# Kernel optimization log

Hardware: AMD Instinct MI355X
Metric: run time of the kernel (lower is better)

## Reference

```python
import jax, jax.numpy as jnp
import numpy as np

N_EMBD = 1024
N_HEAD = 16
HEAD = N_EMBD // N_HEAD


def setup_inputs() -> dict:
    key = jax.random.key(0)
    ks = jax.random.split(key, 6)
    B, S = 4, 2048
    scale = 1.0 / np.sqrt(N_EMBD)
    return {
        "x": jax.random.normal(ks[0], (B, S, N_EMBD), dtype=jnp.float32),
        "Wq": jax.random.normal(ks[1], (N_EMBD, N_EMBD), dtype=jnp.float32) * scale,
        "Wk": jax.random.normal(ks[2], (N_EMBD, N_EMBD), dtype=jnp.float32) * scale,
        "Wv": jax.random.normal(ks[3], (N_EMBD, N_EMBD), dtype=jnp.float32) * scale,
        "Wo": jax.random.normal(ks[4], (N_EMBD, N_EMBD), dtype=jnp.float32) * scale,
        "bo": jnp.zeros((N_EMBD,), dtype=jnp.float32),
    }


def reference(x, Wq, Wk, Wv, Wo, bo):
    B, S, _ = x.shape
    # projections; nn.Linear applies x @ W.T but W is random here, so x @ W is equivalent math
    def split_heads(t):  # (B,S,E) -> (B,H,S,D)
        return t.reshape(B, S, N_HEAD, HEAD).transpose(0, 2, 1, 3)

    q = split_heads(x @ Wq)
    k = split_heads(x @ Wk)
    v = split_heads(x @ Wv)
    scores = jnp.einsum("bhqd,bhkd->bhqk", q, k) * (HEAD ** -0.5)
    causal = jnp.tril(jnp.ones((S, S), dtype=bool))
    scores = jnp.where(causal, scores, -jnp.inf)
    weights = jax.nn.softmax(scores, axis=-1)  # dropout p=0 (eval)
    out = jnp.einsum("bhqk,bhkd->bhqd", weights, v)
    out = out.transpose(0, 2, 1, 3).reshape(B, S, N_EMBD)
    return out @ Wo + bo
```

## Files before the change

### kernel.cpp

```cpp
#include <hip/hip_runtime.h>
#include <hip/hip_bf16.h>

typedef unsigned short u16;
typedef unsigned int u32;
typedef __bf16 bf16x8 __attribute__((ext_vector_type(8)));
typedef float f32x4 __attribute__((ext_vector_type(4)));
typedef u16 u16x8 __attribute__((ext_vector_type(8)));
typedef u16 u16x4 __attribute__((ext_vector_type(4)));

#define NB 4
#define SEQ 2048
#define EMB 1024
#define NHEAD 16
#define DHEAD 64
#define MTOT (NB*SEQ)

static __device__ __forceinline__ u16 f2bf(float f) {
  union { __bf16 h; u16 u; } cv;
  cv.h = (__bf16)f;
  return cv.u;
}

static __device__ __forceinline__ float fexp2(float x) {
  float r;
  asm("v_exp_f32 %0, %1" : "=v"(r) : "v"(x));
  return r;
}

static __device__ __forceinline__ void gload16(const void* g, void* l) {
  __builtin_amdgcn_global_load_lds((const __attribute__((address_space(1))) void*)g,
                                   (__attribute__((address_space(3))) void*)l, 16, 0, 0);
}


__global__ __launch_bounds__(256) void k_cvt_x(const float* __restrict__ in, u16* __restrict__ out) {
  size_t i = (size_t)blockIdx.x * 256 + threadIdx.x;
  const float4* p = (const float4*)in + i * 2;
  float4 a = p[0], b = p[1];
  u16x8 r;
  r[0] = f2bf(a.x); r[1] = f2bf(a.y); r[2] = f2bf(a.z); r[3] = f2bf(a.w);
  r[4] = f2bf(b.x); r[5] = f2bf(b.y); r[6] = f2bf(b.z); r[7] = f2bf(b.w);
  *(u16x8*)(out + i * 8) = r;
}

__global__ __launch_bounds__(256) void k_wtrans(const float* __restrict__ W0, const float* __restrict__ W1,
                                                const float* __restrict__ W2, const float* __restrict__ W3,
                                                u16* __restrict__ O0, u16* __restrict__ O1,
                                                u16* __restrict__ O2, u16* __restrict__ O3) {
  __shared__ float tile[64][65];
  const float* W = blockIdx.z == 0 ? W0 : blockIdx.z == 1 ? W1 : blockIdx.z == 2 ? W2 : W3;
  u16* O       = blockIdx.z == 0 ? O0 : blockIdx.z == 1 ? O1 : blockIdx.z == 2 ? O2 : O3;
  const int c0 = blockIdx.x * 64, r0 = blockIdx.y * 64;
  const int t = threadIdx.x;
  const int tr = t >> 4, tc = (t & 15) * 4;
#pragma unroll
  for (int p = 0; p < 4; p++) {
    int r = tr + p * 16;
    float4 v = *(const float4*)&W[(size_t)(r0 + r) * EMB + c0 + tc];
    tile[r][tc + 0] = v.x; tile[r][tc + 1] = v.y; tile[r][tc + 2] = v.z; tile[r][tc + 3] = v.w;
  }
  __syncthreads();
#pragma unroll
  for (int p = 0; p < 4; p++) {
    int orow = tr + p * 16;
    u16x4 o;
    o[0] = f2bf(tile[tc + 0][orow]); o[1] = f2bf(tile[tc + 1][orow]);
    o[2] = f2bf(tile[tc + 2][orow]); o[3] = f2bf(tile[tc + 3][orow]);
    *(u16x4*)&O[(size_t)(c0 + orow) * EMB + r0 + tc] = o;
  }
}


static __device__ __forceinline__ void gemm_core(const u16* __restrict__ A, const u16* __restrict__ BT,
                                                 int m0, int n0, f32x4 acc[4][4]) {
  __shared__ u16 As[2][128 * 64];
  __shared__ u16 Bs[2][128 * 64];
  const int t = threadIdx.x, l = t & 63, w = t >> 6;
  const int g = l >> 4, q = l & 15;
  const int wm = (w >> 1) * 64, wn = (w & 1) * 64;

  const f32x4 zero4 = {0.f, 0.f, 0.f, 0.f};
#pragma unroll
  for (int mi = 0; mi < 4; mi++)
#pragma unroll
    for (int ni = 0; ni < 4; ni++) acc[mi][ni] = zero4;

  int srow[4], skel[4];
#pragma unroll
  for (int i = 0; i < 4; i++) {
    int row = w * 32 + i * 8 + (l >> 3);
    srow[i] = row; skel[i] = ((l & 7) ^ (row & 7)) * 8;
  }

  auto stage = [&](int k0, int bsel) {
    char* AsB = (char*)As[bsel] + w * 4096;
    char* BsB = (char*)Bs[bsel] + w * 4096;
#pragma unroll
    for (int i = 0; i < 4; i++) {
      gload16(A + (size_t)(m0 + srow[i]) * EMB + k0 + skel[i], AsB + i * 1024);
      gload16(BT + (size_t)(n0 + srow[i]) * EMB + k0 + skel[i], BsB + i * 1024);
    }
  };

  auto compute = [&](int bsel) {
    char* AsB = (char*)As[bsel];
    char* BsB = (char*)Bs[bsel];
#pragma unroll
    for (int kc = 0; kc < 2; kc++) {
      bf16x8 af[4], bfv[4];
#pragma unroll
      for (int mi = 0; mi < 4; mi++) {
        int row = wm + mi * 16 + q;
        af[mi] = *(const bf16x8*)(AsB + row * 128 + (((kc * 4 + g) ^ (row & 7)) << 4));
      }
#pragma unroll
      for (int ni = 0; ni < 4; ni++) {
        int row = wn + ni * 16 + q;
        bfv[ni] = *(const bf16x8*)(BsB + row * 128 + (((kc * 4 + g) ^ (row & 7)) << 4));
      }
      __builtin_amdgcn_s_setprio(1);
#pragma unroll
      for (int mi = 0; mi < 4; mi++)
#pragma unroll
        for (int ni = 0; ni < 4; ni++)
          acc[mi][ni] = __builtin_amdgcn_mfma_f32_16x16x32_bf16(af[mi], bfv[ni], acc[mi][ni], 0, 0, 0);
      __builtin_amdgcn_s_setprio(0);
    }
  };

  stage(0, 0);
  int buf = 0;
  for (int k0 = 64; k0 <= EMB; k0 += 64) {
    const bool pf = (k0 < EMB);
    if (pf) {
      stage(k0, buf ^ 1);
      asm volatile("s_waitcnt vmcnt(8)" ::: "memory");
    } else {
      asm volatile("s_waitcnt vmcnt(0)" ::: "memory");
    }
    __builtin_amdgcn_s_barrier();
    __builtin_amdgcn_sched_barrier(0);
    compute(buf);
    asm volatile("s_waitcnt lgkmcnt(0)" ::: "memory");
    __builtin_amdgcn_s_barrier();
    buf ^= 1;
  }
}

__global__ __launch_bounds__(512, 2) void k_gemm_qkv(const u16* __restrict__ xb, const u16* __restrict__ Wqkv,
                                                     u16* __restrict__ Qb, u16* __restrict__ Kb, u16* __restrict__ Vb) {
  __shared__ u16 As[2][256 * 64];
  __shared__ u16 Bs[2][256 * 64];
  const int t = threadIdx.x, l = t & 63, wid = t >> 6;
  const int g = l >> 4, q = l & 15;
  const int wr = wid >> 2, wc = wid & 3;

  const int wg = blockIdx.x;
  const int c = wg & 7, local = wg >> 3;
  const int idx = c * 48 + local;
  const int ni_ = idx >> 5, mi_ = idx & 31;
  const int m0 = mi_ * 256, n0 = ni_ * 256;

  f32x4 acc[2][2][4][2];
  const f32x4 zero4 = {0.f, 0.f, 0.f, 0.f};
#pragma unroll
  for (int R = 0; R < 2; R++)
#pragma unroll
    for (int C = 0; C < 2; C++)
#pragma unroll
      for (int mi = 0; mi < 4; mi++)
#pragma unroll
        for (int ni = 0; ni < 2; ni++) acc[R][C][mi][ni] = zero4;

  int srow[2], skel[2];
#pragma unroll
  for (int j = 0; j < 2; j++) {
    int row = j * 64 + (t >> 3);
    srow[j] = row; skel[j] = ((t & 7) ^ (row & 7)) * 8;
  }

  auto stageHalf = [&](int op, int half, int tile) {
    if (tile >= 16) return;
    const int kk = tile * 64, d = tile & 1;
    const u16* src = op ? Wqkv : xb;
    const int base = op ? n0 : m0;
    char* dst = (char*)(op ? Bs[d] : As[d]) + half * 16384 + wid * 1024;
#pragma unroll
    for (int j = 0; j < 2; j++)
      gload16(src + (size_t)(base + half * 128 + srow[j]) * EMB + kk + skel[j], dst + j * 8192);
  };

  bf16x8 af[4][2], bf0[2][2], bf1[2][2];
  auto loadA = [&](int R, int d) {
    char* Ab = (char*)As[d];
#pragma unroll
    for (int mi = 0; mi < 4; mi++)
#pragma unroll
      for (int kc = 0; kc < 2; kc++) {
        int row = R * 128 + wr * 64 + mi * 16 + q;
        af[mi][kc] = *(const bf16x8*)(Ab + row * 128 + (((kc * 4 + g) ^ (row & 7)) << 4));
      }
  };
  auto loadB = [&](int C, int d, bf16x8 (&bfv)[2][2]) {
    char* Bb = (char*)Bs[d];
#pragma unroll
    for (int ni = 0; ni < 2; ni++)
#pragma unroll
      for (int kc = 0; kc < 2; kc++) {
        int row = C * 128 + wc * 32 + ni * 16 + q;
        bfv[ni][kc] = *(const bf16x8*)(Bb + row * 128 + (((kc * 4 + g) ^ (row & 7)) << 4));
      }
  };

#define MFMA16(R, C, BF)                                                                   \
  do {                                                                                     \
    __builtin_amdgcn_s_setprio(1);                                                         \
    _Pragma("unroll")                                                                      \
    for (int kc = 0; kc < 2; kc++)                                                         \
      _Pragma("unroll")                                                                    \
      for (int mi = 0; mi < 4; mi++)                                                       \
        _Pragma("unroll")                                                                  \
        for (int ni = 0; ni < 2; ni++)                                                     \
          acc[R][C][mi][ni] = __builtin_amdgcn_mfma_f32_16x16x32_bf16(af[mi][kc], BF[ni][kc], acc[R][C][mi][ni], 0, 0, 0); \
    __builtin_amdgcn_s_setprio(0);                                                         \
  } while (0)

  stageHalf(0, 0, 0); stageHalf(1, 0, 0); stageHalf(1, 1, 0); stageHalf(0, 1, 0);
  stageHalf(0, 0, 1); stageHalf(1, 1, 1);
  asm volatile("s_waitcnt vmcnt(4)" ::: "memory");
  __builtin_amdgcn_s_barrier();
  __builtin_amdgcn_sched_barrier(0);

  for (int kt = 0; kt < 16; ++kt) {
    const int d = kt & 1;
    loadA(0, d); loadB(0, d, bf0);
    stageHalf(0, 1, kt + 1);
    __builtin_amdgcn_s_barrier();
    MFMA16(0, 0, bf0);
    __builtin_amdgcn_s_barrier();
    __builtin_amdgcn_sched_barrier(0);
    loadB(1, d, bf1);
    stageHalf(1, 0, kt + 1);
    __builtin_amdgcn_s_barrier();
    MFMA16(0, 1, bf1);
    __builtin_amdgcn_s_barrier();
    __builtin_amdgcn_sched_barrier(0);
    loadA(1, d);
    stageHalf(0, 0, kt + 2);
    __builtin_amdgcn_s_barrier();
    MFMA16(1, 1, bf1);
    __builtin_amdgcn_s_barrier();
    __builtin_amdgcn_sched_barrier(0);
    stageHalf(1, 1, kt + 2);
    __builtin_amdgcn_s_barrier();
    MFMA16(1, 0, bf0);
    if (kt <= 13)      asm volatile("s_waitcnt vmcnt(4)" ::: "memory");
    else if (kt == 14) asm volatile("s_waitcnt vmcnt(0)" ::: "memory");
    __builtin_amdgcn_s_barrier();
    __builtin_amdgcn_sched_barrier(0);
  }
#undef MFMA16

  const int z = n0 >> 10;
  u16* Out = z == 0 ? Qb : (z == 1 ? Kb : Vb);
  const float scale = z == 0 ? 0.125f * 1.4426950408889634f : 1.0f;

#pragma unroll
  for (int R = 0; R < 2; R++)
#pragma unroll
    for (int C = 0; C < 2; C++)
#pragma unroll
      for (int mi = 0; mi < 4; mi++)
#pragma unroll
        for (int ni = 0; ni < 2; ni++)
#pragma unroll
          for (int jj = 0; jj < 4; jj++) {
            int m = m0 + R * 128 + wr * 64 + mi * 16 + g * 4 + jj;
            int n = n0 + C * 128 + wc * 32 + ni * 16 + q;
            int b = m >> 11, s = m & 2047;
            int col = n & 1023;
            int h = col >> 6, dd = col & 63;
            Out[(((size_t)(b * NHEAD + h)) * SEQ + s) * DHEAD + dd] = f2bf(acc[R][C][mi][ni][jj] * scale);
          }
}

__global__ __launch_bounds__(256) void k_gemm_out(const u16* __restrict__ Ob, const u16* __restrict__ WoT,
                                                  const float* __restrict__ bo, float* __restrict__ out) {
  const int wg = blockIdx.x;
  const int c = wg & 7, local = wg >> 3;
  const int m0 = (local & 63) * 128, n0 = c * 128;

  f32x4 acc[4][4];
  gemm_core(Ob, WoT, m0, n0, acc);

  const int t = threadIdx.x, l = t & 63, w = t >> 6;
  const int g = l >> 4, q = l & 15;
  const int wm = (w >> 1) * 64, wn = (w & 1) * 64;
#pragma unroll
  for (int ni = 0; ni < 4; ni++) {
    int n = n0 + wn + ni * 16 + q;
    float bv = bo[n];
#pragma unroll
    for (int mi = 0; mi < 4; mi++)
#pragma unroll
      for (int jj = 0; jj < 4; jj++) {
        int m = m0 + wm + mi * 16 + g * 4 + jj;
        out[(size_t)m * EMB + n] = acc[mi][ni][jj] + bv;
      }
  }
}

__global__ __launch_bounds__(256, 8) void k_attn(const u16* __restrict__ Qb, const u16* __restrict__ Kb,
                                                 const u16* __restrict__ Vb, u16* __restrict__ Ob) {
  __shared__ u16 Ks[2][64 * 64];
  __shared__ u16 Vt[2][64 * 64];
  const int t = threadIdx.x, l = t & 63, w = t >> 6;
  const int g = l >> 4, q = l & 15;

  const int bid = blockIdx.x;
  const int c = bid & 7, loc = bid >> 3;
  const int bh = c + 8 * (loc >> 5);
  const int qt = 31 - (loc & 31);
  const int b = bh >> 4, h = bh & 15;
  const size_t hb = (size_t)bh * SEQ * DHEAD;
  const float NEG_INF = -__builtin_inff();

  const int q0 = qt * 64;
  const int ntile = qt + 1;

  int krow[2], kel[2];
#pragma unroll
  for (int ii = 0; ii < 2; ii++) {
    int row = w * 16 + ii * 8 + (l >> 3);
    krow[ii] = row; kel[ii] = ((l & 7) ^ (row & 7)) * 8;
  }
  const int kp = t & 31, d0v = (t >> 5) * 8;
  const int r2 = 2 * kp;
  const int sp = 32 * ((r2 >> 4) >> 1) + 8 * ((r2 >> 2) & 3) + 4 * ((r2 >> 4) & 1) + (r2 & 3);

  int olds[2][4], owv[8];
#pragma unroll
  for (int kc = 0; kc < 2; kc++)
#pragma unroll
    for (int kf = 0; kf < 4; kf++) {
      int row = kf * 16 + q;
      olds[kc][kf] = row * 128 + (((kc * 4 + g) ^ (row & 7)) << 4);
    }
#pragma unroll
  for (int ii = 0; ii < 8; ii++) {
    int d = d0v + ii;
    owv[ii] = d * 128 + ((sp * 2) ^ ((d & 7) << 4));
  }

  const u16* kgp0 = Kb + hb + (size_t)krow[0] * DHEAD + kel[0];
  const u16* kgp1 = Kb + hb + (size_t)krow[1] * DHEAD + kel[1];
  const u16* vgp0 = Vb + hb + (size_t)(2 * kp) * DHEAD + d0v;
  const u16* vgp1 = vgp0 + DHEAD;

  auto stageK = [&](const u16* p0, const u16* p1, int bsel) {
    char* dst = (char*)Ks[bsel] + w * 2048;
    gload16(p0, dst);
    gload16(p1, dst + 1024);
  };
  auto writeV = [&](int bsel, const u16x8& v0, const u16x8& v1) {
    char* VtB = (char*)Vt[bsel];
#pragma unroll
    for (int ii = 0; ii < 8; ii++) {
      u32 val = (u32)v0[ii] | ((u32)v1[ii] << 16);
      *(u32*)(VtB + owv[ii]) = val;
    }
  };

  bf16x8 qf[2];
#pragma unroll
  for (int kc = 0; kc < 2; kc++)
    qf[kc] = *(const bf16x8*)(Qb + hb + (size_t)(q0 + w * 16 + q) * DHEAD + kc * 32 + g * 8);
  const int qglob = q0 + w * 16 + q;

  f32x4 o[4];
  const f32x4 zero4 = {0.f, 0.f, 0.f, 0.f};
#pragma unroll
  for (int df = 0; df < 4; df++) o[df] = zero4;
  float m_run = NEG_INF, l_run = 0.f;

  {
    u16x8 v0 = *(const u16x8*)vgp0, v1 = *(const u16x8*)vgp1;
    stageK(kgp0, kgp1, 0);
    writeV(0, v0, v1);
    kgp0 += 4096; kgp1 += 4096; vgp0 += 4096; vgp1 += 4096;
  }
  __syncthreads();

  int buf = 0;
  for (int kt = 0; kt < ntile; ++kt) {
    const int k0 = kt * 64;
    const bool pf = (kt + 1 < ntile);
    u16x8 nv0, nv1;
    if (pf) {
      stageK(kgp0, kgp1, buf ^ 1);
      nv0 = *(const u16x8*)vgp0; nv1 = *(const u16x8*)vgp1;
      kgp0 += 4096; kgp1 += 4096; vgp0 += 4096; vgp1 += 4096;
    }
    const char* KsB = (const char*)Ks[buf];
    const char* VtB = (const char*)Vt[buf];

    f32x4 st[4];
#pragma unroll
    for (int kf = 0; kf < 4; kf++) st[kf] = zero4;
    __builtin_amdgcn_s_setprio(1);
#pragma unroll
    for (int kc = 0; kc < 2; kc++)
#pragma unroll
      for (int kf = 0; kf < 4; kf++) {
        bf16x8 a = *(const bf16x8*)(KsB + olds[kc][kf]);
        st[kf] = __builtin_amdgcn_mfma_f32_16x16x32_bf16(a, qf[kc], st[kf], 0, 0, 0);
      }
    __builtin_amdgcn_s_setprio(0);

    if (kt == ntile - 1) {
#pragma unroll
      for (int kf = 0; kf < 4; kf++)
#pragma unroll
        for (int jj = 0; jj < 4; jj++)
          if (k0 + kf * 16 + g * 4 + jj > qglob) st[kf][jj] = NEG_INF;
    }

    float x0 = fmaxf(fmaxf(st[0][0], st[0][1]), st[0][2]);
    float x1 = fmaxf(fmaxf(st[0][3], st[1][0]), st[1][1]);
    float x2 = fmaxf(fmaxf(st[1][2], st[1][3]), st[2][0]);
    float x3 = fmaxf(fmaxf(st[2][1], st[2][2]), st[2][3]);
    float x4 = fmaxf(fmaxf(st[3][0], st[3][1]), st[3][2]);
    float smax = fmaxf(fmaxf(x0, x1), x2);
    smax = fmaxf(fmaxf(smax, x3), x4);
    smax = fmaxf(smax, st[3][3]);
    smax = fmaxf(smax, __shfl_xor(smax, 16));
    smax = fmaxf(smax, __shfl_xor(smax, 32));

    if (!__all(smax - m_run <= 8.0f)) {
      float mnew = fmaxf(m_run, smax);
      float sc = fexp2(m_run - mnew);
      l_run *= sc;
#pragma unroll
      for (int jj = 0; jj < 4; jj++) {
        float scj = __shfl(sc, g * 4 + jj);
#pragma unroll
        for (int df = 0; df < 4; df++) o[df][jj] *= scj;
      }
      m_run = mnew;
    }

    f32x4 pv[4];
#pragma unroll
    for (int kf = 0; kf < 4; kf++)
#pragma unroll
      for (int jj = 0; jj < 4; jj++)
        pv[kf][jj] = fexp2(st[kf][jj] - m_run);
    f32x4 sv = (pv[0] + pv[1]) + (pv[2] + pv[3]);
    l_run += (sv[0] + sv[1]) + (sv[2] + sv[3]);

    bf16x8 pa[2];
    pa[0] = bf16x8{ (__bf16)pv[0][0], (__bf16)pv[0][1], (__bf16)pv[0][2], (__bf16)pv[0][3],
                    (__bf16)pv[1][0], (__bf16)pv[1][1], (__bf16)pv[1][2], (__bf16)pv[1][3] };
    pa[1] = bf16x8{ (__bf16)pv[2][0], (__bf16)pv[2][1], (__bf16)pv[2][2], (__bf16)pv[2][3],
                    (__bf16)pv[3][0], (__bf16)pv[3][1], (__bf16)pv[3][2], (__bf16)pv[3][3] };

    __builtin_amdgcn_s_setprio(1);
#pragma unroll
    for (int kc = 0; kc < 2; kc++)
#pragma unroll
      for (int df = 0; df < 4; df++) {
        bf16x8 vb = *(const bf16x8*)(VtB + olds[kc][df]);
        o[df] = __builtin_amdgcn_mfma_f32_16x16x32_bf16(pa[kc], vb, o[df], 0, 0, 0);
      }
    __builtin_amdgcn_s_setprio(0);

    if (pf) writeV(buf ^ 1, nv0, nv1);
    __syncthreads();
    buf ^= 1;
  }

  l_run += __shfl_xor(l_run, 16);
  l_run += __shfl_xor(l_run, 32);
  float inv = 1.f / l_run;
#pragma unroll
  for (int jj = 0; jj < 4; jj++) {
    float r = __shfl(inv, g * 4 + jj);
    int s = q0 + w * 16 + g * 4 + jj;
#pragma unroll
    for (int df = 0; df < 4; df++)
      Ob[((size_t)(b * SEQ + s)) * EMB + h * DHEAD + df * 16 + q] = f2bf(o[df][jj] * r);
  }
}


extern "C" void kernel_launch(void* const* d_in, const int* in_sizes, int n_in,
                              void* d_out, int out_size, void* d_ws, size_t ws_size,
                              hipStream_t stream) {
  const float* x  = (const float*)d_in[0];
  const float* Wq = (const float*)d_in[1];
  const float* Wk = (const float*)d_in[2];
  const float* Wv = (const float*)d_in[3];
  const float* Wo = (const float*)d_in[4];
  const float* bo = (const float*)d_in[5];
  float* out = (float*)d_out;

  char* ws = (char*)d_ws;
  u16* xb  = (u16*)(ws);
  u16* WqT = (u16*)(ws + (16u << 20));
  u16* WkT = WqT + (size_t)EMB * EMB;
  u16* WvT = WkT + (size_t)EMB * EMB;
  u16* WoT = WvT + (size_t)EMB * EMB;
  u16* Qb  = (u16*)(ws + (24u << 20));
  u16* Kb  = Qb + (size_t)MTOT * EMB;
  u16* Vb  = Kb + (size_t)MTOT * EMB;
  u16* Ob  = Vb + (size_t)MTOT * EMB;

  k_cvt_x<<<dim3(4096), 256, 0, stream>>>(x, xb);
  k_wtrans<<<dim3(16, 16, 4), 256, 0, stream>>>(Wq, Wk, Wv, Wo, WqT, WkT, WvT, WoT);
  k_gemm_qkv<<<dim3(384), 512, 0, stream>>>(xb, WqT, Qb, Kb, Vb);
  k_attn<<<dim3(2048), 256, 0, stream>>>(Qb, Kb, Vb, Ob);
  k_gemm_out<<<dim3(512), 256, 0, stream>>>(Ob, WoT, bo, out);
}
```

Measured before the change: 189.7 us.

## Process 128-row query blocks with 8 waves sharing each K/V tile

The attention kernel now runs 512-thread blocks, each covering 128 query rows with 8 waves. Every K/V tile staged in shared memory is reused by twice as many query rows, which halves K/V global loads and staging per query. Waves whose rows lie entirely above the diagonal skip compute for the last tile, and masking now covers the last two tiles. In exchange there are fewer, larger blocks, coarser causal load balance, and idle waves on diagonal tiles that still wait at barriers.

```diff
diff --git a/kernel.cpp b/kernel.cpp
--- a/kernel.cpp
+++ b/kernel.cpp
@@ -310,7 +310,7 @@
   }
 }
 
-__global__ __launch_bounds__(256, 8) void k_attn(const u16* __restrict__ Qb, const u16* __restrict__ Kb,
+__global__ __launch_bounds__(512, 8) void k_attn(const u16* __restrict__ Qb, const u16* __restrict__ Kb,
                                                  const u16* __restrict__ Vb, u16* __restrict__ Ob) {
   __shared__ u16 Ks[2][64 * 64];
   __shared__ u16 Vt[2][64 * 64];
@@ -319,26 +319,22 @@
 
   const int bid = blockIdx.x;
   const int c = bid & 7, loc = bid >> 3;
-  const int bh = c + 8 * (loc >> 5);
-  const int qt = 31 - (loc & 31);
+  const int bh = c + 8 * (loc >> 4);
+  const int qblk = 15 - (loc & 15);
   const int b = bh >> 4, h = bh & 15;
   const size_t hb = (size_t)bh * SEQ * DHEAD;
   const float NEG_INF = -__builtin_inff();
 
-  const int q0 = qt * 64;
-  const int ntile = qt + 1;
-
-  int krow[2], kel[2];
-#pragma unroll
-  for (int ii = 0; ii < 2; ii++) {
-    int row = w * 16 + ii * 8 + (l >> 3);
-    krow[ii] = row; kel[ii] = ((l & 7) ^ (row & 7)) * 8;
-  }
-  const int kp = t & 31, d0v = (t >> 5) * 8;
+  const int q0 = qblk * 128;
+  const int ntile = 2 * qblk + 2;
+
+  const int krow = w * 8 + (l >> 3);
+  const int kel = ((l & 7) ^ (krow & 7)) * 8;
+  const int kp = t & 31, db = t >> 5;
   const int r2 = 2 * kp;
   const int sp = 32 * ((r2 >> 4) >> 1) + 8 * ((r2 >> 2) & 3) + 4 * ((r2 >> 4) & 1) + (r2 & 3);
 
-  int olds[2][4], owv[8];
+  int olds[2][4], owv[4];
 #pragma unroll
   for (int kc = 0; kc < 2; kc++)
 #pragma unroll
@@ -347,25 +343,22 @@
       olds[kc][kf] = row * 128 + (((kc * 4 + g) ^ (row & 7)) << 4);
     }
 #pragma unroll
-  for (int ii = 0; ii < 8; ii++) {
-    int d = d0v + ii;
+  for (int ii = 0; ii < 4; ii++) {
+    int d = db * 4 + ii;
     owv[ii] = d * 128 + ((sp * 2) ^ ((d & 7) << 4));
   }
 
-  const u16* kgp0 = Kb + hb + (size_t)krow[0] * DHEAD + kel[0];
-  const u16* kgp1 = Kb + hb + (size_t)krow[1] * DHEAD + kel[1];
-  const u16* vgp0 = Vb + hb + (size_t)(2 * kp) * DHEAD + d0v;
+  const u16* kgp  = Kb + hb + (size_t)krow * DHEAD + kel;
+  const u16* vgp0 = Vb + hb + (size_t)(2 * kp) * DHEAD + db * 4;
   const u16* vgp1 = vgp0 + DHEAD;
 
-  auto stageK = [&](const u16* p0, const u16* p1, int bsel) {
-    char* dst = (char*)Ks[bsel] + w * 2048;
-    gload16(p0, dst);
-    gload16(p1, dst + 1024);
-  };
-  auto writeV = [&](int bsel, const u16x8& v0, const u16x8& v1) {
+  auto stageK = [&](const u16* p, int bsel) {
+    gload16(p, (char*)Ks[bsel] + w * 1024);
+  };
+  auto writeV = [&](int bsel, const u16x4& v0, const u16x4& v1) {
     char* VtB = (char*)Vt[bsel];
 #pragma unroll
-    for (int ii = 0; ii < 8; ii++) {
+    for (int ii = 0; ii < 4; ii++) {
       u32 val = (u32)v0[ii] | ((u32)v1[ii] << 16);
       *(u32*)(VtB + owv[ii]) = val;
     }
@@ -376,6 +369,7 @@
   for (int kc = 0; kc < 2; kc++)
     qf[kc] = *(const bf16x8*)(Qb + hb + (size_t)(q0 + w * 16 + q) * DHEAD + kc * 32 + g * 8);
   const int qglob = q0 + w * 16 + q;
+  const int wave_qmax = q0 + w * 16 + 15;
 
   f32x4 o[4];
   const f32x4 zero4 = {0.f, 0.f, 0.f, 0.f};
@@ -384,10 +378,10 @@
   float m_run = NEG_INF, l_run = 0.f;
 
   {
-    u16x8 v0 = *(const u16x8*)vgp0, v1 = *(const u16x8*)vgp1;
-    stageK(kgp0, kgp1, 0);
+    u16x4 v0 = *(const u16x4*)vgp0, v1 = *(const u16x4*)vgp1;
+    stageK(kgp, 0);
     writeV(0, v0, v1);
-    kgp0 += 4096; kgp1 += 4096; vgp0 += 4096; vgp1 += 4096;
+    kgp += 4096; vgp0 += 4096; vgp1 += 4096;
   }
   __syncthreads();
 
@@ -395,84 +389,86 @@
   for (int kt = 0; kt < ntile; ++kt) {
     const int k0 = kt * 64;
     const bool pf = (kt + 1 < ntile);
-    u16x8 nv0, nv1;
+    u16x4 nv0, nv1;
     if (pf) {
-      stageK(kgp0, kgp1, buf ^ 1);
-      nv0 = *(const u16x8*)vgp0; nv1 = *(const u16x8*)vgp1;
-      kgp0 += 4096; kgp1 += 4096; vgp0 += 4096; vgp1 += 4096;
+      stageK(kgp, buf ^ 1);
+      nv0 = *(const u16x4*)vgp0; nv1 = *(const u16x4*)vgp1;
+      kgp += 4096; vgp0 += 4096; vgp1 += 4096;
     }
     const char* KsB = (const char*)Ks[buf];
     const char* VtB = (const char*)Vt[buf];
 
-    f32x4 st[4];
-#pragma unroll
-    for (int kf = 0; kf < 4; kf++) st[kf] = zero4;
-    __builtin_amdgcn_s_setprio(1);
-#pragma unroll
-    for (int kc = 0; kc < 2; kc++)
-#pragma unroll
-      for (int kf = 0; kf < 4; kf++) {
-        bf16x8 a = *(const bf16x8*)(KsB + olds[kc][kf]);
-        st[kf] = __builtin_amdgcn_mfma_f32_16x16x32_bf16(a, qf[kc], st[kf], 0, 0, 0);
-      }
-    __builtin_amdgcn_s_setprio(0);
-
-    if (kt == ntile - 1) {
+    if (k0 <= wave_qmax) {
+      f32x4 st[4];
+#pragma unroll
+      for (int kf = 0; kf < 4; kf++) st[kf] = zero4;
+      __builtin_amdgcn_s_setprio(1);
+#pragma unroll
+      for (int kc = 0; kc < 2; kc++)
+#pragma unroll
+        for (int kf = 0; kf < 4; kf++) {
+          bf16x8 a = *(const bf16x8*)(KsB + olds[kc][kf]);
+          st[kf] = __builtin_amdgcn_mfma_f32_16x16x32_bf16(a, qf[kc], st[kf], 0, 0, 0);
+        }
+      __builtin_amdgcn_s_setprio(0);
+
+      if (kt >= ntile - 2) {
+#pragma unroll
+        for (int kf = 0; kf < 4; kf++)
+#pragma unroll
+          for (int jj = 0; jj < 4; jj++)
+            if (k0 + kf * 16 + g * 4 + jj > qglob) st[kf][jj] = NEG_INF;
+      }
+
+      float x0 = fmaxf(fmaxf(st[0][0], st[0][1]), st[0][2]);
+      float x1 = fmaxf(fmaxf(st[0][3], st[1][0]), st[1][1]);
+      float x2 = fmaxf(fmaxf(st[1][2], st[1][3]), st[2][0]);
+      float x3 = fmaxf(fmaxf(st[2][1], st[2][2]), st[2][3]);
+      float x4 = fmaxf(fmaxf(st[3][0], st[3][1]), st[3][2]);
+      float smax = fmaxf(fmaxf(x0, x1), x2);
+      smax = fmaxf(fmaxf(smax, x3), x4);
+      smax = fmaxf(smax, st[3][3]);
+      smax = fmaxf(smax, __shfl_xor(smax, 16));
+      smax = fmaxf(smax, __shfl_xor(smax, 32));
+
+      if (!__all(smax - m_run <= 8.0f)) {
+        float mnew = fmaxf(m_run, smax);
+        float sc = fexp2(m_run - mnew);
+        l_run *= sc;
+#pragma unroll
+        for (int jj = 0; jj < 4; jj++) {
+          float scj = __shfl(sc, g * 4 + jj);
+#pragma unroll
+          for (int df = 0; df < 4; df++) o[df][jj] *= scj;
+        }
+        m_run = mnew;
+      }
+
+      f32x4 pv[4];
 #pragma unroll
       for (int kf = 0; kf < 4; kf++)
 #pragma unroll
         for (int jj = 0; jj < 4; jj++)
-          if (k0 + kf * 16 + g * 4 + jj > qglob) st[kf][jj] = NEG_INF;
-    }
-
-    float x0 = fmaxf(fmaxf(st[0][0], st[0][1]), st[0][2]);
-    float x1 = fmaxf(fmaxf(st[0][3], st[1][0]), st[1][1]);
-    float x2 = fmaxf(fmaxf(st[1][2], st[1][3]), st[2][0]);
-    float x3 = fmaxf(fmaxf(st[2][1], st[2][2]), st[2][3]);
-    float x4 = fmaxf(fmaxf(st[3][0], st[3][1]), st[3][2]);
-    float smax = fmaxf(fmaxf(x0, x1), x2);
-    smax = fmaxf(fmaxf(smax, x3), x4);
-    smax = fmaxf(smax, st[3][3]);
-    smax = fmaxf(smax, __shfl_xor(smax, 16));
-    smax = fmaxf(smax, __shfl_xor(smax, 32));
-
-    if (!__all(smax - m_run <= 8.0f)) {
-      float mnew = fmaxf(m_run, smax);
-      float sc = fexp2(m_run - mnew);
-      l_run *= sc;
-#pragma unroll
-      for (int jj = 0; jj < 4; jj++) {
-        float scj = __shfl(sc, g * 4 + jj);
-#pragma unroll
-        for (int df = 0; df < 4; df++) o[df][jj] *= scj;
-      }
-      m_run = mnew;
-    }
-
-    f32x4 pv[4];
-#pragma unroll
-    for (int kf = 0; kf < 4; kf++)
-#pragma unroll
-      for (int jj = 0; jj < 4; jj++)
-        pv[kf][jj] = fexp2(st[kf][jj] - m_run);
-    f32x4 sv = (pv[0] + pv[1]) + (pv[2] + pv[3]);
-    l_run += (sv[0] + sv[1]) + (sv[2] + sv[3]);
-
-    bf16x8 pa[2];
-    pa[0] = bf16x8{ (__bf16)pv[0][0], (__bf16)pv[0][1], (__bf16)pv[0][2], (__bf16)pv[0][3],
-                    (__bf16)pv[1][0], (__bf16)pv[1][1], (__bf16)pv[1][2], (__bf16)pv[1][3] };
-    pa[1] = bf16x8{ (__bf16)pv[2][0], (__bf16)pv[2][1], (__bf16)pv[2][2], (__bf16)pv[2][3],
-                    (__bf16)pv[3][0], (__bf16)pv[3][1], (__bf16)pv[3][2], (__bf16)pv[3][3] };
-
-    __builtin_amdgcn_s_setprio(1);
-#pragma unroll
-    for (int kc = 0; kc < 2; kc++)
-#pragma unroll
-      for (int df = 0; df < 4; df++) {
-        bf16x8 vb = *(const bf16x8*)(VtB + olds[kc][df]);
-        o[df] = __builtin_amdgcn_mfma_f32_16x16x32_bf16(pa[kc], vb, o[df], 0, 0, 0);
-      }
-    __builtin_amdgcn_s_setprio(0);
+          pv[kf][jj] = fexp2(st[kf][jj] - m_run);
+      f32x4 sv = (pv[0] + pv[1]) + (pv[2] + pv[3]);
+      l_run += (sv[0] + sv[1]) + (sv[2] + sv[3]);
+
+      bf16x8 pa[2];
+      pa[0] = bf16x8{ (__bf16)pv[0][0], (__bf16)pv[0][1], (__bf16)pv[0][2], (__bf16)pv[0][3],
+                      (__bf16)pv[1][0], (__bf16)pv[1][1], (__bf16)pv[1][2], (__bf16)pv[1][3] };
+      pa[1] = bf16x8{ (__bf16)pv[2][0], (__bf16)pv[2][1], (__bf16)pv[2][2], (__bf16)pv[2][3],
+                      (__bf16)pv[3][0], (__bf16)pv[3][1], (__bf16)pv[3][2], (__bf16)pv[3][3] };
+
+      __builtin_amdgcn_s_setprio(1);
+#pragma unroll
+      for (int kc = 0; kc < 2; kc++)
+#pragma unroll
+        for (int df = 0; df < 4; df++) {
+          bf16x8 vb = *(const bf16x8*)(VtB + olds[kc][df]);
+          o[df] = __builtin_amdgcn_mfma_f32_16x16x32_bf16(pa[kc], vb, o[df], 0, 0, 0);
+        }
+      __builtin_amdgcn_s_setprio(0);
+    }
 
     if (pf) writeV(buf ^ 1, nv0, nv1);
     __syncthreads();
@@ -518,6 +514,6 @@
   k_cvt_x<<<dim3(4096), 256, 0, stream>>>(x, xb);
   k_wtrans<<<dim3(16, 16, 4), 256, 0, stream>>>(Wq, Wk, Wv, Wo, WqT, WkT, WvT, WoT);
   k_gemm_qkv<<<dim3(384), 512, 0, stream>>>(xb, WqT, Qb, Kb, Vb);
-  k_attn<<<dim3(2048), 256, 0, stream>>>(Qb, Kb, Vb, Ob);
+  k_attn<<<dim3(1024), 512, 0, stream>>>(Qb, Kb, Vb, Ob);
   k_gemm_out<<<dim3(512), 256, 0, stream>>>(Ob, WoT, bo, out);
 }
```

After: 224.3 us. 18.3% more time.
